# Optimization experiments

Hardware: AMD Instinct MI355X
Metric: run time of the kernel (lower is better)

Reference implementation:

```python
import jax, jax.numpy as jnp
import numpy as np

NB, NR = 100000, 200000            # bridge / road node counts
E_BR, E_RB, E_BB = 1000000, 1000000, 500000  # edges per relation
H = 32                             # hidden_channels


def _sage(h_src, h_dst, src, dst, n_dst, Wl, bl, Wr):
    # PyG SAGEConv: lin_l(mean_{j in N(i)} x_j) + lin_r(x_i); lin_r has no bias
    msg = jnp.take(h_src, src, axis=0)                      # [E, H] gather
    s = jax.ops.segment_sum(msg, dst, num_segments=n_dst)   # [n_dst, H] scatter-add
    cnt = jax.ops.segment_sum(jnp.ones((dst.shape[0],), h_src.dtype), dst, num_segments=n_dst)
    mean = s / jnp.maximum(cnt, 1.0)[:, None]                # mean aggregation
    return mean @ Wl + bl + h_dst @ Wr


def setup_inputs():
    key = jax.random.key(0)
    ks = jax.random.split(key, 24)
    n = lambda i, shape, s=0.1: jax.random.normal(ks[i], shape, jnp.float32) * s
    return {
        "x_bridge": n(0, (NB, 16), 1.0),
        "x_road": n(1, (NR, 8), 1.0),
        "src_br": jax.random.randint(ks[2], (E_BR,), 0, NB),
        "dst_br": jax.random.randint(ks[3], (E_BR,), 0, NR),
        "src_rb": jax.random.randint(ks[4], (E_RB,), 0, NR),
        "dst_rb": jax.random.randint(ks[5], (E_RB,), 0, NB),
        "src_bb": jax.random.randint(ks[6], (E_BB,), 0, NB),
        "dst_bb": jax.random.randint(ks[7], (E_BB,), 0, NB),
        "W_enc_b": n(8, (16, H)), "b_enc_b": n(9, (H,)),
        "W_enc_r": n(10, (8, H)), "b_enc_r": n(11, (H,)),
        "Wl_br": n(12, (H, H)), "bl_br": n(13, (H,)), "Wr_br": n(14, (H, H)),
        "Wl_rb": n(15, (H, H)), "bl_rb": n(16, (H,)), "Wr_rb": n(17, (H, H)),
        "Wl_bb": n(18, (H, H)), "bl_bb": n(19, (H,)), "Wr_bb": n(20, (H, H)),
        "Wo": n(21, (H, 1)), "bo": n(22, (1,)),
    }


def reference(x_bridge, x_road, src_br, dst_br, src_rb, dst_rb, src_bb, dst_bb,
              W_enc_b, b_enc_b, W_enc_r, b_enc_r,
              Wl_br, bl_br, Wr_br, Wl_rb, bl_rb, Wr_rb, Wl_bb, bl_bb, Wr_bb,
              Wo, bo):
    # per-node-type encoder + relu
    h_b = jax.nn.relu(x_bridge @ W_enc_b + b_enc_b)          # [NB, H]
    h_r = jax.nn.relu(x_road @ W_enc_r + b_enc_r)            # [NR, H]
    # HeteroConv(aggr='sum'): 'bridge' receives road->bridge and bridge->bridge.
    # (bridge->road output is dead code w.r.t. the returned bridge head; XLA DCEs it.)
    out_b = (_sage(h_r, h_b, src_rb, dst_rb, NB, Wl_rb, bl_rb, Wr_rb)
             + _sage(h_b, h_b, src_bb, dst_bb, NB, Wl_bb, bl_bb, Wr_bb))
    # relu then output Linear on 'bridge'
    return jax.nn.relu(out_b) @ Wo + bo                       # [NB, 1]
```

## Files before the change

kernel.cpp:

```cpp
#include <hip/hip_runtime.h>
#include <hip/hip_fp16.h>

#define H 32
#define TPB 256
#define TPB_P 256
#define TPB2 256
#define EPT 16
#define SLOTS 128
#define CAP 2048
#define MAXBUCK 2048

__global__ void __launch_bounds__(TPB) encoder_kernel(
        const float* __restrict__ x_b, const float* __restrict__ x_r,
        const float* __restrict__ W_b, const float* __restrict__ b_b,
        const float* __restrict__ W_r, const float* __restrict__ b_r,
        __half* __restrict__ h_b16, __half* __restrict__ h_r16,
        int NB, int NR,
        int* __restrict__ gcurp, int NBUCK) {
    int gid = blockIdx.x * TPB + threadIdx.x;
    if (gid < NBUCK) gcurp[gid * 16] = gid * CAP;

    __shared__ float sWb[16][H];
    __shared__ float sWr8[8][H];
    __shared__ float sbb[H];
    __shared__ float sbr[H];
    int t = threadIdx.x;
    for (int i = t; i < 16 * H; i += TPB) ((float*)sWb)[i] = W_b[i];
    for (int i = t; i < 8 * H; i += TPB) ((float*)sWr8)[i] = W_r[i];
    if (t < H) { sbb[t] = b_b[t]; sbr[t] = b_r[t]; }
    __syncthreads();

    long long node = gid;
    if (node < NB) {
        const float4* px = (const float4*)(x_b + node * 16);
        float acc[H];
        #pragma unroll
        for (int j = 0; j < H; ++j) acc[j] = sbb[j];
        #pragma unroll
        for (int c = 0; c < 4; ++c) {
            float4 q = px[c];
            float xs[4] = {q.x, q.y, q.z, q.w};
            #pragma unroll
            for (int u = 0; u < 4; ++u) {
                int k = c * 4 + u;
                #pragma unroll
                for (int j = 0; j < H; ++j)
                    acc[j] = fmaf(xs[u], sWb[k][j], acc[j]);
            }
        }
        __half2 o[H / 2];
        #pragma unroll
        for (int j2 = 0; j2 < H / 2; ++j2)
            o[j2] = __floats2half2_rn(fmaxf(acc[2 * j2], 0.0f), fmaxf(acc[2 * j2 + 1], 0.0f));
        float4* dst = (float4*)(h_b16 + node * H);
        const float4* src = (const float4*)o;
        dst[0] = src[0]; dst[1] = src[1]; dst[2] = src[2]; dst[3] = src[3];
    } else if (node < (long long)NB + NR) {
        long long m = node - NB;
        const float4* px = (const float4*)(x_r + m * 8);
        float acc[H];
        #pragma unroll
        for (int j = 0; j < H; ++j) acc[j] = sbr[j];
        #pragma unroll
        for (int c = 0; c < 2; ++c) {
            float4 q = px[c];
            float xs[4] = {q.x, q.y, q.z, q.w};
            #pragma unroll
            for (int u = 0; u < 4; ++u) {
                int k = c * 4 + u;
                #pragma unroll
                for (int j = 0; j < H; ++j)
                    acc[j] = fmaf(xs[u], sWr8[k][j], acc[j]);
            }
        }
        __half2 o[H / 2];
        #pragma unroll
        for (int j2 = 0; j2 < H / 2; ++j2)
            o[j2] = __floats2half2_rn(fmaxf(acc[2 * j2], 0.0f), fmaxf(acc[2 * j2 + 1], 0.0f));
        float4* dst = (float4*)(h_r16 + m * H);
        const float4* src = (const float4*)o;
        dst[0] = src[0]; dst[1] = src[1]; dst[2] = src[2]; dst[3] = src[3];
    }
}

__global__ void __launch_bounds__(TPB_P) place_kernel(
        const int* __restrict__ src_rb, const int* __restrict__ dst_rb,
        const int* __restrict__ src_bb, const int* __restrict__ dst_bb,
        int* __restrict__ gcurp, int* __restrict__ bins,
        int E_RB, int E_BB, int NB, int NBUCK) {
    __shared__ int lcnt[MAXBUCK];
    __shared__ int wbase[MAXBUCK];
    int t = threadIdx.x;
    for (int i = t; i < MAXBUCK; i += TPB_P) lcnt[i] = 0;
    __syncthreads();
    long long e0 = (long long)blockIdx.x * (TPB_P * EPT);
    long long EA = (long long)E_RB + E_BB;
    int bk[EPT], loc[EPT], pk[EPT];
    #pragma unroll
    for (int j = 0; j < EPT; ++j) {
        long long e = e0 + j * TPB_P + t;
        bk[j] = -1; loc[j] = 0; pk[j] = 0;
        if (e < EA) {
            int s, d;
            if (e < E_RB) { s = src_rb[e]; d = dst_rb[e]; }
            else          { long long e2 = e - E_RB; s = src_bb[e2]; d = NB + dst_bb[e2]; }
            bk[j] = d >> 7;
            pk[j] = (s << 7) | (d & 127);
            loc[j] = atomicAdd(&lcnt[bk[j]], 1);
        }
    }
    __syncthreads();
    for (int i = t; i < NBUCK; i += TPB_P) {
        int c = lcnt[i];
        wbase[i] = c ? atomicAdd(&gcurp[i * 16], c) : 0;
    }
    __syncthreads();
    #pragma unroll
    for (int j = 0; j < EPT; ++j) {
        if (bk[j] >= 0) {
            int gslot = wbase[bk[j]] + loc[j];
            if (gslot < (bk[j] + 1) * CAP)
                bins[gslot] = pk[j];
        }
    }
}

__global__ void __launch_bounds__(TPB2) buildgather_kernel(
        const __half* __restrict__ h_r16, const __half* __restrict__ h_b16,
        const int* __restrict__ bins, const int* __restrict__ gcurp,
        __half* __restrict__ mean16, int NB, int N2) {
    __shared__ int rawbuf[CAP];
    __shared__ int srcbuf[CAP];
    __shared__ int lcnt[SLOTS];
    __shared__ int lbase[SLOTS];
    __shared__ int lcur[SLOTS];
    __shared__ int tmp[SLOTS];
    int t = threadIdx.x;
    int b = blockIdx.x;
    int start = b * CAP;
    int n = gcurp[b * 16] - start;
    if (n > CAP) n = CAP;

    if (t < SLOTS) lcnt[t] = 0;
    __syncthreads();

    for (int i = t; i < n; i += TPB2) {
        int packed = bins[start + i];
        rawbuf[i] = packed;
        atomicAdd(&lcnt[packed & 127], 1);
    }
    __syncthreads();

    if (t < SLOTS) tmp[t] = lcnt[t];
    __syncthreads();
    for (int off = 1; off < SLOTS; off <<= 1) {
        int x = (t >= off && t < SLOTS) ? tmp[t - off] : 0;
        __syncthreads();
        if (t < SLOTS) tmp[t] += x;
        __syncthreads();
    }
    if (t < SLOTS) { lbase[t] = tmp[t] - lcnt[t]; lcur[t] = tmp[t] - lcnt[t]; }
    __syncthreads();

    for (int i = t; i < n; i += TPB2) {
        int packed = rawbuf[i];
        int slot = atomicAdd(&lcur[packed & 127], 1);
        srcbuf[slot] = packed >> 7;
    }
    __syncthreads();

    int lane = t & 15, g = t >> 4;
    long long base_slot = (long long)b << 7;
    for (int sl = g; sl < SLOTS; sl += (TPB2 / 16)) {
        long long gd = base_slot + sl;
        if (gd >= N2) break;
        const __half* __restrict__ hs = (gd < NB) ? h_r16 : h_b16;
        int off = lbase[sl];
        int cnt = lcnt[sl];
        float ax = 0.0f, ay = 0.0f;
        int k = 0;
        for (; k + 4 <= cnt; k += 4) {
            int s0 = srcbuf[off + k];
            int s1 = srcbuf[off + k + 1];
            int s2 = srcbuf[off + k + 2];
            int s3 = srcbuf[off + k + 3];
            float2 f0 = __half22float2(*(const __half2*)(hs + (long long)s0 * H + 2 * lane));
            float2 f1 = __half22float2(*(const __half2*)(hs + (long long)s1 * H + 2 * lane));
            float2 f2 = __half22float2(*(const __half2*)(hs + (long long)s2 * H + 2 * lane));
            float2 f3 = __half22float2(*(const __half2*)(hs + (long long)s3 * H + 2 * lane));
            ax += (f0.x + f1.x) + (f2.x + f3.x);
            ay += (f0.y + f1.y) + (f2.y + f3.y);
        }
        for (; k < cnt; ++k) {
            int s = srcbuf[off + k];
            float2 f = __half22float2(*(const __half2*)(hs + (long long)s * H + 2 * lane));
            ax += f.x; ay += f.y;
        }
        float inv = 1.0f / fmaxf((float)cnt, 1.0f);
        *(__half2*)(mean16 + gd * H + 2 * lane) = __floats2half2_rn(ax * inv, ay * inv);
    }
}

__global__ void __launch_bounds__(TPB) head_kernel(
        const __half* __restrict__ h_b16,
        const __half* __restrict__ mean16,
        const float* __restrict__ Wl_rb,
        const float* __restrict__ bl_rb,
        const float* __restrict__ Wl_bb,
        const float* __restrict__ bl_bb,
        const float* __restrict__ Wr_rb,
        const float* __restrict__ Wr_bb,
        const float* __restrict__ Wo,
        const float* __restrict__ bo,
        float* __restrict__ y, int N) {
    __shared__ float sWl_rb[H][H];
    __shared__ float sWl_bb[H][H];
    __shared__ float sWr[H][H];
    __shared__ float sbl[H];
    __shared__ float sWo[H];
    __shared__ float sbo;

    int t = threadIdx.x;
    for (int i = t; i < H * H; i += blockDim.x) {
        ((float*)sWl_rb)[i] = Wl_rb[i];
        ((float*)sWl_bb)[i] = Wl_bb[i];
        ((float*)sWr)[i]    = Wr_rb[i] + Wr_bb[i];
    }
    if (t < H) {
        sbl[t] = bl_rb[t] + bl_bb[t];
        sWo[t] = Wo[t];
    }
    if (t == 0) sbo = bo[0];
    __syncthreads();

    int node = blockIdx.x * TPB + t;
    if (node >= N) return;

    const float4* pr = (const float4*)(mean16 + (long long)node * H);
    const float4* pb = (const float4*)(mean16 + ((long long)N + node) * H);
    const float4* ph = (const float4*)(h_b16 + (long long)node * H);

    float acc[H];
    #pragma unroll
    for (int j = 0; j < H; ++j) acc[j] = sbl[j];

    #pragma unroll
    for (int c = 0; c < 4; ++c) {
        float4 qr = pr[c];
        float4 qb = pb[c];
        float4 qh = ph[c];
        const __half2* hr = (const __half2*)&qr;
        const __half2* hb = (const __half2*)&qb;
        const __half2* hh = (const __half2*)&qh;
        #pragma unroll
        for (int u = 0; u < 4; ++u) {
            float2 fr = __half22float2(hr[u]);
            float2 fb = __half22float2(hb[u]);
            float2 fh = __half22float2(hh[u]);
            int k0 = c * 8 + u * 2;
            #pragma unroll
            for (int j = 0; j < H; ++j) {
                acc[j] = fmaf(fr.x, sWl_rb[k0][j], acc[j]);
                acc[j] = fmaf(fb.x, sWl_bb[k0][j], acc[j]);
                acc[j] = fmaf(fh.x, sWr[k0][j], acc[j]);
                acc[j] = fmaf(fr.y, sWl_rb[k0 + 1][j], acc[j]);
                acc[j] = fmaf(fb.y, sWl_bb[k0 + 1][j], acc[j]);
                acc[j] = fmaf(fh.y, sWr[k0 + 1][j], acc[j]);
            }
        }
    }

    float out = 0.0f;
    #pragma unroll
    for (int j = 0; j < H; ++j)
        out = fmaf(fmaxf(acc[j], 0.0f), sWo[j], out);
    y[node] = out + sbo;
}

extern "C" void kernel_launch(void* const* d_in, const int* in_sizes, int n_in,
                              void* d_out, int out_size, void* d_ws, size_t ws_size,
                              hipStream_t stream) {
    const float* x_bridge = (const float*)d_in[0];
    const float* x_road   = (const float*)d_in[1];
    const int* src_rb = (const int*)d_in[4];
    const int* dst_rb = (const int*)d_in[5];
    const int* src_bb = (const int*)d_in[6];
    const int* dst_bb = (const int*)d_in[7];
    const float* W_enc_b = (const float*)d_in[8];
    const float* b_enc_b = (const float*)d_in[9];
    const float* W_enc_r = (const float*)d_in[10];
    const float* b_enc_r = (const float*)d_in[11];
    const float* Wl_rb = (const float*)d_in[15];
    const float* bl_rb = (const float*)d_in[16];
    const float* Wr_rb = (const float*)d_in[17];
    const float* Wl_bb = (const float*)d_in[18];
    const float* bl_bb = (const float*)d_in[19];
    const float* Wr_bb = (const float*)d_in[20];
    const float* Wo = (const float*)d_in[21];
    const float* bo = (const float*)d_in[22];
    float* y = (float*)d_out;

    const int NB = in_sizes[0] / 16;
    const int NR = in_sizes[1] / 8;
    const int E_RB = in_sizes[4];
    const int E_BB = in_sizes[6];
    const int N2 = 2 * NB;
    const long long E_ALL = (long long)E_RB + E_BB;
    const int NBUCK = (N2 + SLOTS - 1) / SLOTS;

    char* wp = (char*)d_ws;
    __half* h_r16  = (__half*)wp; wp += (size_t)NR * H * sizeof(__half);
    __half* h_b16  = (__half*)wp; wp += (size_t)NB * H * sizeof(__half);
    __half* mean16 = (__half*)wp; wp += (size_t)N2 * H * sizeof(__half);
    int* bins  = (int*)wp;       wp += (size_t)NBUCK * CAP * sizeof(int);
    int* gcurp = (int*)wp;       wp += (size_t)NBUCK * 16 * sizeof(int);

    {
        long long nodes = (long long)NB + NR;
        int blocks = (int)((nodes + TPB - 1) / TPB);
        encoder_kernel<<<blocks, TPB, 0, stream>>>(x_bridge, x_road,
                                                   W_enc_b, b_enc_b, W_enc_r, b_enc_r,
                                                   h_b16, h_r16, NB, NR, gcurp, NBUCK);
    }

    int nWGe = (int)((E_ALL + (TPB_P * EPT) - 1) / (TPB_P * EPT));
    place_kernel<<<nWGe, TPB_P, 0, stream>>>(src_rb, dst_rb, src_bb, dst_bb,
                                             gcurp, bins, E_RB, E_BB, NB, NBUCK);

    buildgather_kernel<<<NBUCK, TPB2, 0, stream>>>(h_r16, h_b16, bins, gcurp,
                                                   mean16, NB, N2);

    head_kernel<<<(NB + TPB - 1) / TPB, TPB, 0, stream>>>(h_b16, mean16,
                                                  Wl_rb, bl_rb, Wl_bb, bl_bb,
                                                  Wr_rb, Wr_bb, Wo, bo, y, NB);
}
```

Baseline: 104.7 us.

## Replace per-bucket counting sort with LDS atomic accumulation in gather kernel

The gather kernel no longer runs the per-bucket histogram, prefix scan and scatter that sorted edges by destination before summing. Each 16-lane group now reads packed edges straight from the bins, loads the source features, and adds them into a padded shared-memory accumulator with float atomics, counting degrees with integer atomics. This removes the scan's many barriers and the two shared-memory passes over the edges, and allows more loads in flight. The cost is heavy LDS atomic traffic with contention on popular destinations, and float summation order that is no longer deterministic.

```diff
diff --git a/kernel.cpp b/kernel.cpp
--- a/kernel.cpp
+++ b/kernel.cpp
@@ -129,75 +129,56 @@
         const __half* __restrict__ h_r16, const __half* __restrict__ h_b16,
         const int* __restrict__ bins, const int* __restrict__ gcurp,
         __half* __restrict__ mean16, int NB, int N2) {
-    __shared__ int rawbuf[CAP];
-    __shared__ int srcbuf[CAP];
-    __shared__ int lcnt[SLOTS];
-    __shared__ int lbase[SLOTS];
-    __shared__ int lcur[SLOTS];
-    __shared__ int tmp[SLOTS];
+    __shared__ float acc[SLOTS * 33];
+    __shared__ int   scnt[SLOTS];
     int t = threadIdx.x;
     int b = blockIdx.x;
     int start = b * CAP;
     int n = gcurp[b * 16] - start;
     if (n > CAP) n = CAP;
 
-    if (t < SLOTS) lcnt[t] = 0;
-    __syncthreads();
-
-    for (int i = t; i < n; i += TPB2) {
-        int packed = bins[start + i];
-        rawbuf[i] = packed;
-        atomicAdd(&lcnt[packed & 127], 1);
-    }
-    __syncthreads();
-
-    if (t < SLOTS) tmp[t] = lcnt[t];
-    __syncthreads();
-    for (int off = 1; off < SLOTS; off <<= 1) {
-        int x = (t >= off && t < SLOTS) ? tmp[t - off] : 0;
-        __syncthreads();
-        if (t < SLOTS) tmp[t] += x;
-        __syncthreads();
-    }
-    if (t < SLOTS) { lbase[t] = tmp[t] - lcnt[t]; lcur[t] = tmp[t] - lcnt[t]; }
-    __syncthreads();
-
-    for (int i = t; i < n; i += TPB2) {
-        int packed = rawbuf[i];
-        int slot = atomicAdd(&lcur[packed & 127], 1);
-        srcbuf[slot] = packed >> 7;
-    }
+    for (int i = t; i < SLOTS * 33; i += TPB2) acc[i] = 0.0f;
+    if (t < SLOTS) scnt[t] = 0;
     __syncthreads();
 
     int lane = t & 15, g = t >> 4;
     long long base_slot = (long long)b << 7;
-    for (int sl = g; sl < SLOTS; sl += (TPB2 / 16)) {
+    for (int e = g; e < n; e += 64) {
+        int pk[4];
+        #pragma unroll
+        for (int u = 0; u < 4; ++u) {
+            int idx = e + u * 16;
+            pk[u] = (idx < n) ? bins[start + idx] : -1;
+        }
+        float2 f[4];
+        #pragma unroll
+        for (int u = 0; u < 4; ++u) {
+            if (pk[u] >= 0) {
+                int s = pk[u] >> 7;
+                long long gd0 = base_slot + (pk[u] & 127);
+                const __half* __restrict__ hs = (gd0 < NB) ? h_r16 : h_b16;
+                f[u] = __half22float2(*(const __half2*)(hs + (long long)s * H + 2 * lane));
+            }
+        }
+        #pragma unroll
+        for (int u = 0; u < 4; ++u) {
+            if (pk[u] >= 0) {
+                int dloc = pk[u] & 127;
+                atomicAdd(&acc[dloc * 33 + 2 * lane], f[u].x);
+                atomicAdd(&acc[dloc * 33 + 2 * lane + 1], f[u].y);
+                if (lane == 0) atomicAdd(&scnt[dloc], 1);
+            }
+        }
+    }
+    __syncthreads();
+
+    for (int sl = g; sl < SLOTS; sl += 16) {
         long long gd = base_slot + sl;
         if (gd >= N2) break;
-        const __half* __restrict__ hs = (gd < NB) ? h_r16 : h_b16;
-        int off = lbase[sl];
-        int cnt = lcnt[sl];
-        float ax = 0.0f, ay = 0.0f;
-        int k = 0;
-        for (; k + 4 <= cnt; k += 4) {
-            int s0 = srcbuf[off + k];
-            int s1 = srcbuf[off + k + 1];
-            int s2 = srcbuf[off + k + 2];
-            int s3 = srcbuf[off + k + 3];
-            float2 f0 = __half22float2(*(const __half2*)(hs + (long long)s0 * H + 2 * lane));
-            float2 f1 = __half22float2(*(const __half2*)(hs + (long long)s1 * H + 2 * lane));
-            float2 f2 = __half22float2(*(const __half2*)(hs + (long long)s2 * H + 2 * lane));
-            float2 f3 = __half22float2(*(const __half2*)(hs + (long long)s3 * H + 2 * lane));
-            ax += (f0.x + f1.x) + (f2.x + f3.x);
-            ay += (f0.y + f1.y) + (f2.y + f3.y);
-        }
-        for (; k < cnt; ++k) {
-            int s = srcbuf[off + k];
-            float2 f = __half22float2(*(const __half2*)(hs + (long long)s * H + 2 * lane));
-            ax += f.x; ay += f.y;
-        }
-        float inv = 1.0f / fmaxf((float)cnt, 1.0f);
-        *(__half2*)(mean16 + gd * H + 2 * lane) = __floats2half2_rn(ax * inv, ay * inv);
+        float inv = 1.0f / fmaxf((float)scnt[sl], 1.0f);
+        float ax = acc[sl * 33 + 2 * lane] * inv;
+        float ay = acc[sl * 33 + 2 * lane + 1] * inv;
+        *(__half2*)(mean16 + gd * H + 2 * lane) = __floats2half2_rn(ax, ay);
     }
 }
 
```

Measured after the change: 369.3 us. 253% more time.
